# Kernel tuning notes

Measured on AMD Instinct MI355X. Metric: run time of the kernel, lower is better.

The kernel has to match this reference:

```python
import jax, jax.numpy as jnp
import numpy as np

N, NODES, DIN, HID, M, OUT_FE = 8192, 20000, 768, 256, 4096, 50


def setup_inputs() -> dict:
    key = jax.random.key(0)
    ks = jax.random.split(key, 12)
    s = 0.02  # small init scale to keep tanh in its linear-ish range
    return {
        "t": jax.random.normal(ks[0], (N, DIN), jnp.float32),
        "AGE_inx": jax.random.normal(ks[1], (NODES, DIN), jnp.float32),
        "Endx": jax.random.randint(ks[2], (M,), 0, NODES, jnp.int32),
        "W_age": jax.random.normal(ks[3], (DIN, DIN), jnp.float32) * s,
        "b_age": jnp.zeros((DIN,), jnp.float32),
        "W_prjT": jax.random.normal(ks[4], (HID, DIN), jnp.float32) * s,
        "b_prjT": jnp.zeros((HID,), jnp.float32),
        "W_prjL": jax.random.normal(ks[5], (HID, DIN), jnp.float32) * s,
        "b_prjL": jnp.zeros((HID,), jnp.float32),
        "outW": jax.random.normal(ks[6], (M, HID), jnp.float32) * s,
        "outb": jax.random.normal(ks[7], (M,), jnp.float32) * s,
        "W_fc3": jax.random.normal(ks[8], (OUT_FE, HID), jnp.float32) * s,
        "b_fc3": jnp.zeros((OUT_FE,), jnp.float32),
    }


def _lintrans(x, W, b):
    # AGE LinTrans: Linear -> per-row min-max scale -> L2 normalize
    z = x @ W.T + b                                   # [NODES, 768]
    zmin = jnp.min(z, axis=1, keepdims=True)
    zmax = jnp.max(z, axis=1, keepdims=True)
    z = (z - zmin) / (zmax - zmin)
    norm = jnp.sqrt(jnp.sum(z * z, axis=1, keepdims=True))
    return z / jnp.maximum(norm, 1e-12)


def reference(t, AGE_inx, Endx, W_age, b_age, W_prjT, b_prjT,
              W_prjL, b_prjL, outW, outb, W_fc3, b_fc3):
    AGE_E = _lintrans(AGE_inx, W_age, b_age)          # [NODES, 768]
    h = jnp.tanh(t @ W_prjT.T + b_prjT)               # [N, 256]
    E = jnp.tanh(AGE_E[Endx] @ W_prjL.T + b_prjL)     # [M, 256]
    # sum_d h[n,d]*E[m,d]*outW[m,d] == h @ (E*outW).T  (avoids [N,M,256] blowup)
    o_c = h @ (E * outW).T + outb                     # [N, M]
    o_f = h @ W_fc3.T + b_fc3                         # [N, OUT_FE]
    return (o_c, o_f)
```

## Files before the change

### kernel.cpp

```cpp
#include <hip/hip_runtime.h>
#include <hip/hip_bf16.h>
#include <cstdint>
#include <cstddef>

typedef __hip_bfloat16 bf16;
typedef __attribute__((ext_vector_type(4))) float f32x4;
typedef __attribute__((ext_vector_type(8))) short s16x8;

__device__ __forceinline__ void gload_lds16(const void* g, void* l) {
    __builtin_amdgcn_global_load_lds(
        (const __attribute__((address_space(1))) unsigned int*)g,
        (__attribute__((address_space(3))) unsigned int*)l,
        16, 0, 0);
}

__global__ __launch_bounds__(256)
void cvt_f32_bf16(const float* __restrict__ src, bf16* __restrict__ dst, int n)
{
    int i = (blockIdx.x * 256 + threadIdx.x) * 4;
    if (i + 3 < n) {
        float4 v = *(const float4*)(src + i);
        dst[i + 0] = __float2bfloat16(v.x);
        dst[i + 1] = __float2bfloat16(v.y);
        dst[i + 2] = __float2bfloat16(v.z);
        dst[i + 3] = __float2bfloat16(v.w);
    }
}

__global__ __launch_bounds__(256)
void gather_cvt(const float* __restrict__ src, const int* __restrict__ idx,
                bf16* __restrict__ dst)
{
    int row = blockIdx.x;
    int r = idx[row];
    const float* s = src + (size_t)r * 768;
    bf16* d = dst + (size_t)row * 768;
    int c = threadIdx.x * 4;
    if (c < 768) {
        float4 v = *(const float4*)(s + c);
        d[c + 0] = __float2bfloat16(v.x);
        d[c + 1] = __float2bfloat16(v.y);
        d[c + 2] = __float2bfloat16(v.z);
        d[c + 3] = __float2bfloat16(v.w);
    }
}

template<int TANH, int MULW, int F32OUT, int NGUARD>
__global__ __launch_bounds__(256)
void gemm_bt(const bf16* __restrict__ A, const bf16* __restrict__ B,
             const float* __restrict__ bias, const float* __restrict__ Mul,
             void* __restrict__ Cout, int M, int N, int K, int ldc)
{
    __shared__ short sA[128 * 64];
    __shared__ short sB[128 * 64];

    const int tid  = threadIdx.x;
    const int lane = tid & 63;
    const int wave = tid >> 6;
    const int bm = blockIdx.y, bn = blockIdx.x;
    const int wr = wave >> 1, wc = wave & 1;
    const int l15 = lane & 15, quad = lane >> 4;

    f32x4 acc[4][4];
#pragma unroll
    for (int i = 0; i < 4; ++i)
#pragma unroll
        for (int j = 0; j < 4; ++j)
            acc[i][j] = (f32x4){0.f, 0.f, 0.f, 0.f};

    for (int kt = 0; kt < K; kt += 64) {
#pragma unroll
        for (int j = 0; j < 4; ++j) {
            int S   = (wave * 4 + j) * 64 + lane;
            int row = S >> 3;
            int cc  = (S & 7) ^ (row & 7);
            gload_lds16(A + (size_t)(bm * 128 + row) * K + kt + cc * 8, &sA[S * 8]);
        }
#pragma unroll
        for (int j = 0; j < 4; ++j) {
            int S   = (wave * 4 + j) * 64 + lane;
            int row = S >> 3;
            int cc  = (S & 7) ^ (row & 7);
            int ng  = bn * 128 + row;
            if (NGUARD) ng = (ng < N) ? ng : (N - 1);
            gload_lds16(B + (size_t)ng * K + kt + cc * 8, &sB[S * 8]);
        }
        asm volatile("s_waitcnt vmcnt(0)" ::: "memory");
        __syncthreads();

#pragma unroll
        for (int ks = 0; ks < 2; ++ks) {
            s16x8 afr[4], bfr[4];
#pragma unroll
            for (int i = 0; i < 4; ++i) {
                int r = wr * 64 + i * 16 + l15;
                int q = ks * 4 + quad;
                afr[i] = *(const s16x8*)&sA[(r * 8 + (q ^ (r & 7))) * 8];
            }
#pragma unroll
            for (int j = 0; j < 4; ++j) {
                int r = wc * 64 + j * 16 + l15;
                int q = ks * 4 + quad;
                bfr[j] = *(const s16x8*)&sB[(r * 8 + (q ^ (r & 7))) * 8];
            }
#pragma unroll
            for (int i = 0; i < 4; ++i)
#pragma unroll
                for (int j = 0; j < 4; ++j)
                    acc[i][j] = __builtin_amdgcn_mfma_f32_16x16x32_bf16(
                        afr[i], bfr[j], acc[i][j], 0, 0, 0);
        }
        __syncthreads();
    }

#pragma unroll
    for (int j = 0; j < 4; ++j) {
        int colg = bn * 128 + wc * 64 + j * 16 + l15;
        if (NGUARD && colg >= N) continue;
        float bv = bias[colg];
#pragma unroll
        for (int i = 0; i < 4; ++i) {
            int row0 = bm * 128 + wr * 64 + i * 16 + quad * 4;
#pragma unroll
            for (int r = 0; r < 4; ++r) {
                float v = acc[i][j][r] + bv;
                if (TANH) v = tanhf(v);
                if (MULW) v *= Mul[(size_t)(row0 + r) * N + colg];
                if (F32OUT)
                    ((float*)Cout)[(size_t)(row0 + r) * ldc + colg] = v;
                else
                    ((bf16*)Cout)[(size_t)(row0 + r) * ldc + colg] = __float2bfloat16(v);
            }
        }
    }
}

__global__ __launch_bounds__(256)
void lintrans_k(const float* __restrict__ z, bf16* __restrict__ out)
{
    __shared__ float rmin[4], rmax[4], rsum[4];
    const int row  = blockIdx.x;
    const int tid  = threadIdx.x;
    const int lane = tid & 63;
    const int wave = tid >> 6;
    const float* zr = z + (size_t)row * 768;

    float v0 = zr[tid], v1 = zr[tid + 256], v2 = zr[tid + 512];
    float mn = fminf(fminf(v0, v1), v2);
    float mx = fmaxf(fmaxf(v0, v1), v2);
#pragma unroll
    for (int o = 32; o > 0; o >>= 1) {
        mn = fminf(mn, __shfl_down(mn, o));
        mx = fmaxf(mx, __shfl_down(mx, o));
    }
    if (lane == 0) { rmin[wave] = mn; rmax[wave] = mx; }
    __syncthreads();
    float bmn = fminf(fminf(rmin[0], rmin[1]), fminf(rmin[2], rmin[3]));
    float bmx = fmaxf(fmaxf(rmax[0], rmax[1]), fmaxf(rmax[2], rmax[3]));
    float sc  = 1.f / (bmx - bmn);
    v0 = (v0 - bmn) * sc; v1 = (v1 - bmn) * sc; v2 = (v2 - bmn) * sc;
    float s = v0 * v0 + v1 * v1 + v2 * v2;
#pragma unroll
    for (int o = 32; o > 0; o >>= 1) s += __shfl_down(s, o);
    if (lane == 0) rsum[wave] = s;
    __syncthreads();
    float tot = rsum[0] + rsum[1] + rsum[2] + rsum[3];
    float inv = 1.f / fmaxf(sqrtf(tot), 1e-12f);
    out[(size_t)row * 768 + tid]       = __float2bfloat16(v0 * inv);
    out[(size_t)row * 768 + tid + 256] = __float2bfloat16(v1 * inv);
    out[(size_t)row * 768 + tid + 512] = __float2bfloat16(v2 * inv);
}

extern "C" void kernel_launch(void* const* d_in, const int* in_sizes, int n_in,
                              void* d_out, int out_size, void* d_ws, size_t ws_size,
                              hipStream_t stream)
{
    (void)in_sizes; (void)n_in; (void)out_size; (void)ws_size;

    const float* t_in   = (const float*)d_in[0];
    const float* AGEinx = (const float*)d_in[1];
    const int*   Endx   = (const int*)  d_in[2];
    const float* W_age  = (const float*)d_in[3];
    const float* b_age  = (const float*)d_in[4];
    const float* W_prjT = (const float*)d_in[5];
    const float* b_prjT = (const float*)d_in[6];
    const float* W_prjL = (const float*)d_in[7];
    const float* b_prjL = (const float*)d_in[8];
    const float* outW   = (const float*)d_in[9];
    const float* outb   = (const float*)d_in[10];
    const float* W_fc3  = (const float*)d_in[11];
    const float* b_fc3  = (const float*)d_in[12];

    char* ws = (char*)d_ws;
    size_t off = 0;
    float* z    = (float*)(ws + off);
    bf16*  h    = (bf16*)(ws + off);
    off += (size_t)4096 * 768 * 4;
    bf16* tb    = (bf16*)(ws + off); off += (size_t)8192 * 768 * 2;
    bf16* AGEg  = (bf16*)(ws + off); off += (size_t)4096 * 768 * 2;
    bf16* Wageb = (bf16*)(ws + off); off += (size_t)768 * 768 * 2;
    bf16* WpTb  = (bf16*)(ws + off); off += (size_t)256 * 768 * 2;
    bf16* WpLb  = (bf16*)(ws + off); off += (size_t)256 * 768 * 2;
    bf16* Wfc3b = (bf16*)(ws + off); off += (size_t)50 * 256 * 2 + 64;
    bf16* AGE_E = (bf16*)(ws + off); off += (size_t)4096 * 768 * 2;
    bf16* E2    = (bf16*)(ws + off); off += (size_t)4096 * 256 * 2;

    float* o_c = (float*)d_out;
    float* o_f = o_c + (size_t)8192 * 4096;

    cvt_f32_bf16<<<6144, 256, 0, stream>>>(t_in,   tb,    8192 * 768);
    cvt_f32_bf16<<<576,  256, 0, stream>>>(W_age,  Wageb, 768 * 768);
    cvt_f32_bf16<<<192,  256, 0, stream>>>(W_prjT, WpTb,  256 * 768);
    cvt_f32_bf16<<<192,  256, 0, stream>>>(W_prjL, WpLb,  256 * 768);
    cvt_f32_bf16<<<13,   256, 0, stream>>>(W_fc3,  Wfc3b, 50 * 256);
    gather_cvt  <<<4096, 256, 0, stream>>>(AGEinx, Endx,  AGEg);

    gemm_bt<0,0,1,0><<<dim3(6, 32), 256, 0, stream>>>(
        AGEg, Wageb, b_age, nullptr, z, 4096, 768, 768, 768);
    lintrans_k<<<4096, 256, 0, stream>>>(z, AGE_E);
    gemm_bt<1,1,0,0><<<dim3(2, 32), 256, 0, stream>>>(
        AGE_E, WpLb, b_prjL, outW, E2, 4096, 256, 768, 256);
    gemm_bt<1,0,0,0><<<dim3(2, 64), 256, 0, stream>>>(
        tb, WpTb, b_prjT, nullptr, h, 8192, 256, 768, 256);
    gemm_bt<0,0,1,0><<<dim3(32, 64), 256, 0, stream>>>(
        h, E2, outb, nullptr, o_c, 8192, 4096, 256, 4096);
    gemm_bt<0,0,1,1><<<dim3(1, 64), 256, 0, stream>>>(
        h, Wfc3b, b_fc3, nullptr, o_f, 8192, 50, 256, 50);
}
```

Baseline: 342.8 us.

## Fuse fp32-to-bf16 conversion and gather into GEMM loads, merge GEMM launches

Removes the separate conversion and gather kernels by having the GEMM tile loaders read fp32 (optionally via the Endx index) and convert to bf16 while storing into LDS. Independent GEMMs (AGE linear + t projection, o_c + o_f) are merged into single launches that dispatch on block index, cutting the launch count from 12 to 4. The trade-off is that fp32 operands now go through registers instead of the direct global-to-LDS path, which doubles global read bytes per tile and adds conversion work inside the K loop.

```diff
diff --git a/kernel.cpp b/kernel.cpp
--- a/kernel.cpp
+++ b/kernel.cpp
@@ -14,53 +14,43 @@
         16, 0, 0);
 }
 
-__global__ __launch_bounds__(256)
-void cvt_f32_bf16(const float* __restrict__ src, bf16* __restrict__ dst, int n)
-{
-    int i = (blockIdx.x * 256 + threadIdx.x) * 4;
-    if (i + 3 < n) {
-        float4 v = *(const float4*)(src + i);
-        dst[i + 0] = __float2bfloat16(v.x);
-        dst[i + 1] = __float2bfloat16(v.y);
-        dst[i + 2] = __float2bfloat16(v.z);
-        dst[i + 3] = __float2bfloat16(v.w);
-    }
-}
-
-__global__ __launch_bounds__(256)
-void gather_cvt(const float* __restrict__ src, const int* __restrict__ idx,
-                bf16* __restrict__ dst)
-{
-    int row = blockIdx.x;
-    int r = idx[row];
-    const float* s = src + (size_t)r * 768;
-    bf16* d = dst + (size_t)row * 768;
-    int c = threadIdx.x * 4;
-    if (c < 768) {
-        float4 v = *(const float4*)(s + c);
-        d[c + 0] = __float2bfloat16(v.x);
-        d[c + 1] = __float2bfloat16(v.y);
-        d[c + 2] = __float2bfloat16(v.z);
-        d[c + 3] = __float2bfloat16(v.w);
-    }
-}
-
-template<int TANH, int MULW, int F32OUT, int NGUARD>
-__global__ __launch_bounds__(256)
-void gemm_bt(const bf16* __restrict__ A, const bf16* __restrict__ B,
-             const float* __restrict__ bias, const float* __restrict__ Mul,
-             void* __restrict__ Cout, int M, int N, int K, int ldc)
-{
-    __shared__ short sA[128 * 64];
-    __shared__ short sB[128 * 64];
-
+__device__ __forceinline__ short f2bs(float x) {
+    bf16 h = __float2bfloat16(x);
+    return *reinterpret_cast<short*>(&h);
+}
+
+template<int TANH, int MULW, int F32OUT, int NGUARD, int ASRC, int BSRC>
+__device__ __forceinline__ void gemm_body(
+    short* __restrict__ sA, short* __restrict__ sB,
+    int bm, int bn,
+    const void* __restrict__ Aptr, const void* __restrict__ Bptr,
+    const int* __restrict__ gidx,
+    const float* __restrict__ bias, const float* __restrict__ Mul,
+    void* __restrict__ Cout, int M, int N, int K, int ldc)
+{
     const int tid  = threadIdx.x;
     const int lane = tid & 63;
     const int wave = tid >> 6;
-    const int bm = blockIdx.y, bn = blockIdx.x;
     const int wr = wave >> 1, wc = wave & 1;
     const int l15 = lane & 15, quad = lane >> 4;
 
+    int    slot[4];
+    size_t a_off[4], b_off[4];
+#pragma unroll
+    for (int j = 0; j < 4; ++j) {
+        int S   = (wave * 4 + j) * 64 + lane;
+        int row = S >> 3;
+        int cc  = (S & 7) ^ (row & 7);
+        slot[j] = S * 8;
+        if (ASRC == 2)
+            a_off[j] = (size_t)gidx[bm * 128 + row] * K + cc * 8;
+        else
+            a_off[j] = (size_t)(bm * 128 + row) * K + cc * 8;
+        int ng = bn * 128 + row;
+        if (NGUARD) ng = (ng < N) ? ng : (N - 1);
+        b_off[j] = (size_t)ng * K + cc * 8;
+    }
+
     f32x4 acc[4][4];
 #pragma unroll
     for (int i = 0; i < 4; ++i)
@@ -71,21 +61,34 @@
     for (int kt = 0; kt < K; kt += 64) {
 #pragma unroll
         for (int j = 0; j < 4; ++j) {
-            int S   = (wave * 4 + j) * 64 + lane;
-            int row = S >> 3;
-            int cc  = (S & 7) ^ (row & 7);
-            gload_lds16(A + (size_t)(bm * 128 + row) * K + kt + cc * 8, &sA[S * 8]);
+            if (ASRC == 0) {
+                gload_lds16((const bf16*)Aptr + a_off[j] + kt, &sA[slot[j]]);
+            } else {
+                const float* s = (const float*)Aptr + a_off[j] + kt;
+                float4 u = *(const float4*)s;
+                float4 v = *(const float4*)(s + 4);
+                s16x8 p;
+                p[0] = f2bs(u.x); p[1] = f2bs(u.y); p[2] = f2bs(u.z); p[3] = f2bs(u.w);
+                p[4] = f2bs(v.x); p[5] = f2bs(v.y); p[6] = f2bs(v.z); p[7] = f2bs(v.w);
+                *(s16x8*)&sA[slot[j]] = p;
+            }
         }
 #pragma unroll
         for (int j = 0; j < 4; ++j) {
-            int S   = (wave * 4 + j) * 64 + lane;
-            int row = S >> 3;
-            int cc  = (S & 7) ^ (row & 7);
-            int ng  = bn * 128 + row;
-            if (NGUARD) ng = (ng < N) ? ng : (N - 1);
-            gload_lds16(B + (size_t)ng * K + kt + cc * 8, &sB[S * 8]);
-        }
-        asm volatile("s_waitcnt vmcnt(0)" ::: "memory");
+            if (BSRC == 0) {
+                gload_lds16((const bf16*)Bptr + b_off[j] + kt, &sB[slot[j]]);
+            } else {
+                const float* s = (const float*)Bptr + b_off[j] + kt;
+                float4 u = *(const float4*)s;
+                float4 v = *(const float4*)(s + 4);
+                s16x8 p;
+                p[0] = f2bs(u.x); p[1] = f2bs(u.y); p[2] = f2bs(u.z); p[3] = f2bs(u.w);
+                p[4] = f2bs(v.x); p[5] = f2bs(v.y); p[6] = f2bs(v.z); p[7] = f2bs(v.w);
+                *(s16x8*)&sB[slot[j]] = p;
+            }
+        }
+        if (ASRC == 0 || BSRC == 0)
+            asm volatile("s_waitcnt vmcnt(0)" ::: "memory");
         __syncthreads();
 
 #pragma unroll
@@ -132,6 +135,61 @@
                     ((bf16*)Cout)[(size_t)(row0 + r) * ldc + colg] = __float2bfloat16(v);
             }
         }
+    }
+}
+
+__global__ __launch_bounds__(256)
+void mm_zh(const float* __restrict__ AGEinx, const int* __restrict__ Endx,
+           const float* __restrict__ W_age, const float* __restrict__ b_age,
+           float* __restrict__ z,
+           const float* __restrict__ t, const float* __restrict__ W_prjT,
+           const float* __restrict__ b_prjT, bf16* __restrict__ h)
+{
+    __shared__ short sA[128 * 64];
+    __shared__ short sB[128 * 64];
+    int b = blockIdx.x;
+    if (b < 192) {
+        gemm_body<0, 0, 1, 0, 2, 1>(sA, sB, b / 6, b % 6,
+                                    AGEinx, W_age, Endx, b_age, nullptr,
+                                    z, 4096, 768, 768, 768);
+    } else {
+        int b2 = b - 192;
+        gemm_body<1, 0, 0, 0, 1, 1>(sA, sB, b2 / 2, b2 % 2,
+                                    t, W_prjT, nullptr, b_prjT, nullptr,
+                                    h, 8192, 256, 768, 256);
+    }
+}
+
+__global__ __launch_bounds__(256)
+void mm_e2(const bf16* __restrict__ AGE_E, const float* __restrict__ W_prjL,
+           const float* __restrict__ b_prjL, const float* __restrict__ outW,
+           bf16* __restrict__ E2)
+{
+    __shared__ short sA[128 * 64];
+    __shared__ short sB[128 * 64];
+    gemm_body<1, 1, 0, 0, 0, 1>(sA, sB, blockIdx.y, blockIdx.x,
+                                AGE_E, W_prjL, nullptr, b_prjL, outW,
+                                E2, 4096, 256, 768, 256);
+}
+
+__global__ __launch_bounds__(256)
+void mm_out(const bf16* __restrict__ h, const bf16* __restrict__ E2,
+            const float* __restrict__ outb, float* __restrict__ o_c,
+            const float* __restrict__ W_fc3, const float* __restrict__ b_fc3,
+            float* __restrict__ o_f)
+{
+    __shared__ short sA[128 * 64];
+    __shared__ short sB[128 * 64];
+    int b = blockIdx.x;
+    if (b < 2048) {
+        gemm_body<0, 0, 1, 0, 0, 0>(sA, sB, b / 32, b % 32,
+                                    h, E2, nullptr, outb, nullptr,
+                                    o_c, 8192, 4096, 256, 4096);
+    } else {
+        int b2 = b - 2048;
+        gemm_body<0, 0, 1, 1, 0, 1>(sA, sB, b2, 0,
+                                    h, W_fc3, nullptr, b_fc3, nullptr,
+                                    o_f, 8192, 50, 256, 50);
     }
 }
 
@@ -193,37 +251,17 @@
 
     char* ws = (char*)d_ws;
     size_t off = 0;
-    float* z    = (float*)(ws + off);
-    bf16*  h    = (bf16*)(ws + off);
-    off += (size_t)4096 * 768 * 4;
-    bf16* tb    = (bf16*)(ws + off); off += (size_t)8192 * 768 * 2;
-    bf16* AGEg  = (bf16*)(ws + off); off += (size_t)4096 * 768 * 2;
-    bf16* Wageb = (bf16*)(ws + off); off += (size_t)768 * 768 * 2;
-    bf16* WpTb  = (bf16*)(ws + off); off += (size_t)256 * 768 * 2;
-    bf16* WpLb  = (bf16*)(ws + off); off += (size_t)256 * 768 * 2;
-    bf16* Wfc3b = (bf16*)(ws + off); off += (size_t)50 * 256 * 2 + 64;
-    bf16* AGE_E = (bf16*)(ws + off); off += (size_t)4096 * 768 * 2;
-    bf16* E2    = (bf16*)(ws + off); off += (size_t)4096 * 256 * 2;
+    float* z     = (float*)(ws + off); off += (size_t)4096 * 768 * 4;
+    bf16*  h     = (bf16*) (ws + off); off += (size_t)8192 * 256 * 2;
+    bf16*  AGE_E = (bf16*) (ws + off); off += (size_t)4096 * 768 * 2;
+    bf16*  E2    = (bf16*) (ws + off); off += (size_t)4096 * 256 * 2;
 
     float* o_c = (float*)d_out;
     float* o_f = o_c + (size_t)8192 * 4096;
 
-    cvt_f32_bf16<<<6144, 256, 0, stream>>>(t_in,   tb,    8192 * 768);
-    cvt_f32_bf16<<<576,  256, 0, stream>>>(W_age,  Wageb, 768 * 768);
-    cvt_f32_bf16<<<192,  256, 0, stream>>>(W_prjT, WpTb,  256 * 768);
-    cvt_f32_bf16<<<192,  256, 0, stream>>>(W_prjL, WpLb,  256 * 768);
-    cvt_f32_bf16<<<13,   256, 0, stream>>>(W_fc3,  Wfc3b, 50 * 256);
-    gather_cvt  <<<4096, 256, 0, stream>>>(AGEinx, Endx,  AGEg);
-
-    gemm_bt<0,0,1,0><<<dim3(6, 32), 256, 0, stream>>>(
-        AGEg, Wageb, b_age, nullptr, z, 4096, 768, 768, 768);
+    mm_zh<<<320, 256, 0, stream>>>(AGEinx, Endx, W_age, b_age, z,
+                                   t_in, W_prjT, b_prjT, h);
     lintrans_k<<<4096, 256, 0, stream>>>(z, AGE_E);
-    gemm_bt<1,1,0,0><<<dim3(2, 32), 256, 0, stream>>>(
-        AGE_E, WpLb, b_prjL, outW, E2, 4096, 256, 768, 256);
-    gemm_bt<1,0,0,0><<<dim3(2, 64), 256, 0, stream>>>(
-        tb, WpTb, b_prjT, nullptr, h, 8192, 256, 768, 256);
-    gemm_bt<0,0,1,0><<<dim3(32, 64), 256, 0, stream>>>(
-        h, E2, outb, nullptr, o_c, 8192, 4096, 256, 4096);
-    gemm_bt<0,0,1,1><<<dim3(1, 64), 256, 0, stream>>>(
-        h, Wfc3b, b_fc3, nullptr, o_f, 8192, 50, 256, 50);
-}
+    mm_e2<<<dim3(2, 32), 256, 0, stream>>>(AGE_E, W_prjL, b_prjL, outW, E2);
+    mm_out<<<2112, 256, 0, stream>>>(h, E2, outb, o_c, W_fc3, b_fc3, o_f);
+}
```

Measured after the change: 344.5 us. No clear change (+0.5%).
